# Performance work log

Hardware: AMD Instinct MI355X
Metric: run time of the kernel (lower is better)

Reference implementation:

```python
import jax, jax.numpy as jnp
import numpy as np

EPS = 1e-20

def setup_inputs() -> dict:
    key = jax.random.key(0)
    k1, k2 = jax.random.split(key)
    x = jax.random.normal(k1, (8192, 4096), dtype=jnp.float32)
    weight = jax.random.normal(k2, (4096, 4096), dtype=jnp.float32)  # [out, in]
    return {"x": x, "weight": weight}

def reference(x, weight):
    # Binarize activations and weights with sign(v + eps), then matmul.
    xb = jnp.sign(x + EPS)
    wb = jnp.sign(weight + EPS)
    return jnp.matmul(xb, wb.T)  # [N, out]
```

## Files before the change

kernel.cpp:

```cpp
#include <hip/hip_runtime.h>
#include <stdint.h>

#define EPSF 1e-20f

typedef __attribute__((ext_vector_type(4))) int i32x4;
typedef __attribute__((ext_vector_type(8))) int i32x8;
typedef __attribute__((ext_vector_type(16))) float f32x16;


__global__ __launch_bounds__(256)
void bin_fp4_kernel(const float4* __restrict__ src, uint32_t* __restrict__ dst,
                    int n8) {
    int base = blockIdx.x * 1024 + threadIdx.x;
#pragma unroll
    for (int j = 0; j < 4; ++j) {
        int idx = base + j * 256;
        if (idx < n8) {
            float4 v0 = src[2 * idx];
            float4 v1 = src[2 * idx + 1];
            uint32_t w = 0;
            w |= ((v0.x < -EPSF) ? 0xAu : 0x2u);
            w |= ((v0.y < -EPSF) ? 0xAu : 0x2u) << 4;
            w |= ((v0.z < -EPSF) ? 0xAu : 0x2u) << 8;
            w |= ((v0.w < -EPSF) ? 0xAu : 0x2u) << 12;
            w |= ((v1.x < -EPSF) ? 0xAu : 0x2u) << 16;
            w |= ((v1.y < -EPSF) ? 0xAu : 0x2u) << 20;
            w |= ((v1.z < -EPSF) ? 0xAu : 0x2u) << 24;
            w |= ((v1.w < -EPSF) ? 0xAu : 0x2u) << 28;
            dst[idx] = w;
        }
    }
}

#define GM 128
#define GN 128
#define GKB 128
#define KB4 2048

#define SCALE_ONE 0x7F7F7F7Fu

__global__ __launch_bounds__(256, 3)
void fp4mfma_gemm(const char* __restrict__ x4, const char* __restrict__ w4,
                  float* __restrict__ out) {
    __shared__ char xs[GM * GKB];
    __shared__ char wsh[GN * GKB];

    const int t = threadIdx.x;
    const int lane = t & 63;
    const int wave = t >> 6;
    const int wm = (wave >> 1) * 64;
    const int wn = (wave & 1) * 64;
    const int row0 = blockIdx.y * GM;
    const int col0 = blockIdx.x * GN;
    const int lrow = lane & 31;
    const int half = lane >> 5;

    f32x16 acc[2][2];
#pragma unroll
    for (int r = 0; r < 2; ++r)
#pragma unroll
        for (int c = 0; c < 2; ++c)
#pragma unroll
            for (int e = 0; e < 16; ++e) acc[r][c][e] = 0.0f;

    i32x8 a[2], b[2];
#pragma unroll
    for (int r = 0; r < 2; ++r)
#pragma unroll
        for (int e = 0; e < 8; ++e) { a[r][e] = 0; b[r][e] = 0; }

    for (int kb = 0; kb < 2048; kb += GKB) {
        __syncthreads();
#pragma unroll
        for (int j = 0; j < 4; ++j) {
            int c = j * 256 + t;
            int row = c >> 3;
            int q = c & 7;
            int qg = q ^ (row & 7);
            const char* srcx = x4 + (size_t)(row0 + row) * KB4 + kb + qg * 16;
            __builtin_amdgcn_global_load_lds((const uint32_t*)srcx,
                                             (uint32_t*)(xs + c * 16), 16, 0, 0);
            const char* srcw = w4 + (size_t)(col0 + row) * KB4 + kb + qg * 16;
            __builtin_amdgcn_global_load_lds((const uint32_t*)srcw,
                                             (uint32_t*)(wsh + c * 16), 16, 0, 0);
        }
        __syncthreads();

#pragma unroll
        for (int m = 0; m < 4; ++m) {
            int g = 2 * m + half;
#pragma unroll
            for (int r = 0; r < 2; ++r) {
                int row = wm + r * 32 + lrow;
                int qs = g ^ (row & 7);
                i32x4 av = *(const i32x4*)(xs + row * GKB + qs * 16);
                a[r][0] = av[0]; a[r][1] = av[1];
                a[r][2] = av[2]; a[r][3] = av[3];
            }
#pragma unroll
            for (int c = 0; c < 2; ++c) {
                int col = wn + c * 32 + lrow;
                int qs = g ^ (col & 7);
                i32x4 bv = *(const i32x4*)(wsh + col * GKB + qs * 16);
                b[c][0] = bv[0]; b[c][1] = bv[1];
                b[c][2] = bv[2]; b[c][3] = bv[3];
            }
#pragma unroll
            for (int r = 0; r < 2; ++r)
#pragma unroll
                for (int c = 0; c < 2; ++c)
                    acc[r][c] = __builtin_amdgcn_mfma_scale_f32_32x32x64_f8f6f4(
                        a[r], b[c], acc[r][c],
                        4, 4,
                        0, SCALE_ONE,
                        0, SCALE_ONE);
        }
    }

#pragma unroll
    for (int r = 0; r < 2; ++r)
#pragma unroll
        for (int c = 0; c < 2; ++c)
#pragma unroll
            for (int e = 0; e < 16; ++e) {
                int rr = row0 + wm + r * 32 + (e & 3) + 8 * (e >> 2) + 4 * half;
                int cc = col0 + wn + c * 32 + lrow;
                out[(size_t)rr * 4096 + cc] = acc[r][c][e];
            }
}


__global__ __launch_bounds__(256)
void binarize_kernel(const float* __restrict__ src,
                     unsigned long long* __restrict__ dst, int n256) {
    int wave = blockIdx.x * 4 + (threadIdx.x >> 6);
    if (wave >= n256) return;
    int lane = threadIdx.x & 63;
    const float4* p = (const float4*)(src + (size_t)wave * 256);
    float4 v = p[lane];
    unsigned long long m0 = __ballot(v.x < -EPSF);
    unsigned long long m1 = __ballot(v.y < -EPSF);
    unsigned long long m2 = __ballot(v.z < -EPSF);
    unsigned long long m3 = __ballot(v.w < -EPSF);
    if (lane < 4) {
        unsigned long long m = (lane == 0) ? m0 : (lane == 1) ? m1
                             : (lane == 2) ? m2 : m3;
        dst[(size_t)wave * 4 + lane] = m;
    }
}

#define BM 128
#define BN 128
#define CHUNK_Q 8
#define NCHUNK 4
#define LDSS 9

__global__ __launch_bounds__(256, 2)
void bingemm_kernel(const uint4* __restrict__ xb, const uint4* __restrict__ wb,
                    float* __restrict__ out) {
    __shared__ uint4 xsl[BM * LDSS];
    __shared__ uint4 wsl[BN * LDSS];

    const int t  = threadIdx.x;
    const int tx = t & 15;
    const int ty = t >> 4;
    const int row0 = blockIdx.y * BM;
    const int col0 = blockIdx.x * BN;

    int acc[8][8];
#pragma unroll
    for (int a = 0; a < 8; ++a)
#pragma unroll
        for (int b = 0; b < 8; ++b) acc[a][b] = 0;

    const int srow = t >> 3;
    const int sq   = t & 7;

    for (int c = 0; c < NCHUNK; ++c) {
        __syncthreads();
#pragma unroll
        for (int k = 0; k < 4; ++k) {
            int r = srow + 32 * k;
            xsl[r * LDSS + sq] = xb[(size_t)(row0 + r) * 32 + c * CHUNK_Q + sq];
            wsl[r * LDSS + sq] = wb[(size_t)(col0 + r) * 32 + c * CHUNK_Q + sq];
        }
        __syncthreads();

#pragma unroll
        for (int q = 0; q < CHUNK_Q; ++q) {
            uint4 xq[8], wq[8];
#pragma unroll
            for (int ri = 0; ri < 8; ++ri)
                xq[ri] = xsl[(ty + 16 * ri) * LDSS + q];
#pragma unroll
            for (int cj = 0; cj < 8; ++cj)
                wq[cj] = wsl[(tx + 16 * cj) * LDSS + q];
#pragma unroll
            for (int ri = 0; ri < 8; ++ri)
#pragma unroll
                for (int cj = 0; cj < 8; ++cj) {
                    acc[ri][cj] += __builtin_popcount(xq[ri].x ^ wq[cj].x);
                    acc[ri][cj] += __builtin_popcount(xq[ri].y ^ wq[cj].y);
                    acc[ri][cj] += __builtin_popcount(xq[ri].z ^ wq[cj].z);
                    acc[ri][cj] += __builtin_popcount(xq[ri].w ^ wq[cj].w);
                }
        }
    }

#pragma unroll
    for (int ri = 0; ri < 8; ++ri) {
        size_t i = row0 + ty + 16 * ri;
#pragma unroll
        for (int cj = 0; cj < 8; ++cj) {
            int j = col0 + tx + 16 * cj;
            out[i * 4096 + j] = (float)(4096 - 2 * acc[ri][cj]);
        }
    }
}

extern "C" void kernel_launch(void* const* d_in, const int* in_sizes, int n_in,
                              void* d_out, int out_size, void* d_ws, size_t ws_size,
                              hipStream_t stream) {
    const float* x = (const float*)d_in[0];
    const float* w = (const float*)d_in[1];
    float* out = (float*)d_out;

    const int M = 8192, N = 4096, K = 4096;
    const size_t need_fp4 = ((size_t)M * K + (size_t)N * K) / 2;

    if (ws_size >= need_fp4) {
        char* x4 = (char*)d_ws;
        char* w4 = x4 + (size_t)M * K / 2;

        int n8x = (M * K) / 8;
        int n8w = (N * K) / 8;
        bin_fp4_kernel<<<n8x / 1024, 256, 0, stream>>>(
            (const float4*)x, (uint32_t*)x4, n8x);
        bin_fp4_kernel<<<n8w / 1024, 256, 0, stream>>>(
            (const float4*)w, (uint32_t*)w4, n8w);

        dim3 grid(N / GN, M / GM);
        fp4mfma_gemm<<<grid, 256, 0, stream>>>(x4, w4, out);
    } else {
        uint32_t* xbits = (uint32_t*)d_ws;
        uint32_t* wbits = xbits + (size_t)M * (K / 32);

        binarize_kernel<<<(M * K) / 1024, 256, 0, stream>>>(
            x, (unsigned long long*)xbits, (M * K) / 256);
        binarize_kernel<<<(N * K) / 1024, 256, 0, stream>>>(
            w, (unsigned long long*)wbits, (N * K) / 256);

        dim3 grid(N / BN, M / BM);
        bingemm_kernel<<<grid, 256, 0, stream>>>(
            (const uint4*)xbits, (const uint4*)wbits, out);
    }
}
```

Before: 330.1 us.

## Use 256x256 FP4 MFMA tiles with double-buffered LDS prefetch

Replaces the 128x128 FP4 GEMM with a 512-thread, 256x256-tile kernel. Each wave now computes a 128x64 sub-tile and the kernel double-buffers K tiles in LDS, issuing global-to-LDS loads for the next tile between MFMA groups. It precomputes address offsets and raises wave priority around the MFMA block. This aims to reduce global traffic per FLOP and hide load latency. In exchange it uses 128KB of LDS per block and more accumulator registers, which lowers occupancy.

```diff
diff --git a/kernel.cpp b/kernel.cpp
--- a/kernel.cpp
+++ b/kernel.cpp
@@ -32,81 +32,104 @@
     }
 }
 
-#define GM 128
-#define GN 128
-#define GKB 128
-#define KB4 2048
-
 #define SCALE_ONE 0x7F7F7F7Fu
 
-__global__ __launch_bounds__(256, 3)
-void fp4mfma_gemm(const char* __restrict__ x4, const char* __restrict__ w4,
-                  float* __restrict__ out) {
-    __shared__ char xs[GM * GKB];
-    __shared__ char wsh[GN * GKB];
+__global__ __launch_bounds__(512, 2)
+void fp4mfma_gemm256(const char* __restrict__ x4, const char* __restrict__ w4,
+                     float* __restrict__ out) {
+    __shared__ char lds[2][65536];
 
     const int t = threadIdx.x;
     const int lane = t & 63;
     const int wave = t >> 6;
-    const int wm = (wave >> 1) * 64;
-    const int wn = (wave & 1) * 64;
-    const int row0 = blockIdx.y * GM;
-    const int col0 = blockIdx.x * GN;
+    const int wm = (wave >> 2) * 128;
+    const int wn = (wave & 3) * 64;
+    const int row0 = blockIdx.y * 256;
+    const int col0 = blockIdx.x * 256;
     const int lrow = lane & 31;
     const int half = lane >> 5;
 
-    f32x16 acc[2][2];
-#pragma unroll
-    for (int r = 0; r < 2; ++r)
+    const char* xbase = x4 + (size_t)row0 * 2048;
+    const char* wbase = w4 + (size_t)col0 * 2048;
+
+    int goff[4], loff[4];
+#pragma unroll
+    for (int j = 0; j < 4; ++j) {
+        int cid = j * 512 + t;
+        int crow = cid >> 3;
+        int cqg = (cid & 7) ^ (crow & 7);
+        goff[j] = crow * 2048 + cqg * 16;
+        loff[j] = cid * 16;
+    }
+
+    f32x16 acc[4][2];
+#pragma unroll
+    for (int r = 0; r < 4; ++r)
 #pragma unroll
         for (int c = 0; c < 2; ++c)
 #pragma unroll
             for (int e = 0; e < 16; ++e) acc[r][c][e] = 0.0f;
 
-    i32x8 a[2], b[2];
-#pragma unroll
-    for (int r = 0; r < 2; ++r)
-#pragma unroll
-        for (int e = 0; e < 8; ++e) { a[r][e] = 0; b[r][e] = 0; }
-
-    for (int kb = 0; kb < 2048; kb += GKB) {
-        __syncthreads();
-#pragma unroll
-        for (int j = 0; j < 4; ++j) {
-            int c = j * 256 + t;
-            int row = c >> 3;
-            int q = c & 7;
-            int qg = q ^ (row & 7);
-            const char* srcx = x4 + (size_t)(row0 + row) * KB4 + kb + qg * 16;
-            __builtin_amdgcn_global_load_lds((const uint32_t*)srcx,
-                                             (uint32_t*)(xs + c * 16), 16, 0, 0);
-            const char* srcw = w4 + (size_t)(col0 + row) * KB4 + kb + qg * 16;
-            __builtin_amdgcn_global_load_lds((const uint32_t*)srcw,
-                                             (uint32_t*)(wsh + c * 16), 16, 0, 0);
-        }
-        __syncthreads();
+    i32x8 a[4], b[2];
+#pragma unroll
+    for (int r = 0; r < 4; ++r)
+#pragma unroll
+        for (int e = 0; e < 8; ++e) a[r][e] = 0;
+#pragma unroll
+    for (int c = 0; c < 2; ++c)
+#pragma unroll
+        for (int e = 0; e < 8; ++e) b[c][e] = 0;
+
+    const int laneA = (wm + lrow) * 128;
+    const int laneB = (wn + lrow) * 128;
+
+#pragma unroll
+    for (int j = 0; j < 4; ++j) {
+        __builtin_amdgcn_global_load_lds((const uint32_t*)(xbase + goff[j]),
+                                         (uint32_t*)(&lds[0][0] + loff[j]),
+                                         16, 0, 0);
+        __builtin_amdgcn_global_load_lds((const uint32_t*)(wbase + goff[j]),
+                                         (uint32_t*)(&lds[0][0] + 32768 + loff[j]),
+                                         16, 0, 0);
+    }
+    __syncthreads();
+
+    for (int kt = 0; kt < 16; ++kt) {
+        const int cur = kt & 1;
+        const char* curA = &lds[cur][0];
+        const char* curB = &lds[cur][0] + 32768;
+        char* nxt = &lds[cur ^ 1][0];
+        const int kbn = (kt + 1) * 128;
+        const bool stage = (kt < 15);
 
 #pragma unroll
         for (int m = 0; m < 4; ++m) {
-            int g = 2 * m + half;
-#pragma unroll
-            for (int r = 0; r < 2; ++r) {
-                int row = wm + r * 32 + lrow;
-                int qs = g ^ (row & 7);
-                i32x4 av = *(const i32x4*)(xs + row * GKB + qs * 16);
+            if (stage) {
+                __builtin_amdgcn_global_load_lds(
+                    (const uint32_t*)(xbase + goff[m] + kbn),
+                    (uint32_t*)(nxt + loff[m]), 16, 0, 0);
+                __builtin_amdgcn_global_load_lds(
+                    (const uint32_t*)(wbase + goff[m] + kbn),
+                    (uint32_t*)(nxt + 32768 + loff[m]), 16, 0, 0);
+            }
+
+            const int qs16 = (((2 * m + half) ^ (lrow & 7)) << 4);
+#pragma unroll
+            for (int r = 0; r < 4; ++r) {
+                i32x4 av = *(const i32x4*)(curA + laneA + r * 4096 + qs16);
                 a[r][0] = av[0]; a[r][1] = av[1];
                 a[r][2] = av[2]; a[r][3] = av[3];
             }
 #pragma unroll
             for (int c = 0; c < 2; ++c) {
-                int col = wn + c * 32 + lrow;
-                int qs = g ^ (col & 7);
-                i32x4 bv = *(const i32x4*)(wsh + col * GKB + qs * 16);
+                i32x4 bv = *(const i32x4*)(curB + laneB + c * 4096 + qs16);
                 b[c][0] = bv[0]; b[c][1] = bv[1];
                 b[c][2] = bv[2]; b[c][3] = bv[3];
             }
-#pragma unroll
-            for (int r = 0; r < 2; ++r)
+
+            __builtin_amdgcn_s_setprio(1);
+#pragma unroll
+            for (int r = 0; r < 4; ++r)
 #pragma unroll
                 for (int c = 0; c < 2; ++c)
                     acc[r][c] = __builtin_amdgcn_mfma_scale_f32_32x32x64_f8f6f4(
@@ -114,11 +137,13 @@
                         4, 4,
                         0, SCALE_ONE,
                         0, SCALE_ONE);
-        }
-    }
-
-#pragma unroll
-    for (int r = 0; r < 2; ++r)
+            __builtin_amdgcn_s_setprio(0);
+        }
+        __syncthreads();
+    }
+
+#pragma unroll
+    for (int r = 0; r < 4; ++r)
 #pragma unroll
         for (int c = 0; c < 2; ++c)
 #pragma unroll
@@ -239,8 +264,8 @@
         bin_fp4_kernel<<<n8w / 1024, 256, 0, stream>>>(
             (const float4*)w, (uint32_t*)w4, n8w);
 
-        dim3 grid(N / GN, M / GM);
-        fp4mfma_gemm<<<grid, 256, 0, stream>>>(x4, w4, out);
+        dim3 grid(N / 256, M / 256);
+        fp4mfma_gemm256<<<grid, 512, 0, stream>>>(x4, w4, out);
     } else {
         uint32_t* xbits = (uint32_t*)d_ws;
         uint32_t* wbits = xbits + (size_t)M * (K / 32);
```

Result: no change. 329.2 us (-0.3%).
